# Performance work log

Hardware: AMD Instinct MI355X
Metric: run time of the kernel (lower is better)

The kernel has to match this reference:

```python
import jax, jax.numpy as jnp
import numpy as np

B, L, D_IN, D_OUT = 4, 2048, 4096, 4096


def setup_inputs() -> dict:
    key = jax.random.key(0)
    k1, k2, k3, k4 = jax.random.split(key, 4)
    x = jax.random.normal(k1, (B, L, D_IN), dtype=jnp.float32)
    # base weight stored transposed as [in, out], like self.base = base.T
    base = jax.random.normal(k2, (D_IN, D_OUT), dtype=jnp.float32) * 0.02
    # binary delta sign mask in {0, 1}, stored transposed [in, out]
    mask = jax.random.randint(k3, (D_IN, D_OUT), 0, 2).astype(jnp.int32)
    # coeff = mean(|finetune - base|); a small positive scalar
    coeff = jax.random.uniform(k4, (1,), dtype=jnp.float32) * 0.01
    return {"x": x, "base": base, "coeff": coeff, "mask": mask}


def reference(x, base, coeff, mask):
    # Original: x @ base.T_stored + coeff * (x @ repeated_mask)
    # (t_coeff * x) @ mask == t_coeff * (x @ mask); we avoid materializing the
    # per-batch repeated mask since broadcasting the [in, out] mask is equivalent.
    m = mask.astype(x.dtype)            # {0,1} dequantized mask, [in, out]
    c = coeff[0].astype(x.dtype)
    return jnp.einsum('bld,de->ble', x, base) + c * jnp.einsum('bld,de->ble', x, m)
```

## Files before the change

### kernel.cpp

```cpp
#include <hip/hip_runtime.h>
#include <hip/hip_bf16.h>
#include <stdint.h>

#define DIN 4096
#define DOUT 4096
#define BK 64
#define NT (DIN / BK)

typedef __attribute__((ext_vector_type(8))) short short8;
typedef __attribute__((ext_vector_type(8))) unsigned short ushort8;
typedef __attribute__((ext_vector_type(4))) float f32x4;

__device__ inline unsigned short f2bf(float f) {
    union { float f; unsigned u; } v; v.f = f;
    unsigned r = v.u + 0x7fffu + ((v.u >> 16) & 1u);
    return (unsigned short)(r >> 16);
}

__global__ void cvt_x_kernel(const float* __restrict__ x, ushort* __restrict__ xb, long n8) {
    long i = (long)blockIdx.x * blockDim.x + threadIdx.x;
    if (i >= n8) return;
    const float4* p = (const float4*)(x + i * 8);
    float4 v0 = p[0], v1 = p[1];
    ushort8 o;
    o[0] = f2bf(v0.x); o[1] = f2bf(v0.y); o[2] = f2bf(v0.z); o[3] = f2bf(v0.w);
    o[4] = f2bf(v1.x); o[5] = f2bf(v1.y); o[6] = f2bf(v1.z); o[7] = f2bf(v1.w);
    *(ushort8*)(xb + i * 8) = o;
}

__global__ void make_wt_kernel(const float* __restrict__ base, const int* __restrict__ mask,
                               const float* __restrict__ coeff, ushort* __restrict__ wt) {
    __shared__ float tile[64][65];
    const float c = coeff[0];
    const int t = threadIdx.x;
    const int bd = blockIdx.x >> 6;
    const int be = blockIdx.x & 63;
    const int d0 = bd * 64, e0 = be * 64;
#pragma unroll
    for (int i = 0; i < 4; ++i) {
        int idx = i * 256 + t;
        int r = idx >> 4;
        int c4 = (idx & 15) << 2;
        const float4 bv = *(const float4*)(base + (size_t)(d0 + r) * DOUT + e0 + c4);
        const int4  mv = *(const int4*)(mask + (size_t)(d0 + r) * DOUT + e0 + c4);
        tile[r][c4 + 0] = bv.x + c * (float)mv.x;
        tile[r][c4 + 1] = bv.y + c * (float)mv.y;
        tile[r][c4 + 2] = bv.z + c * (float)mv.z;
        tile[r][c4 + 3] = bv.w + c * (float)mv.w;
    }
    __syncthreads();
#pragma unroll
    for (int i = 0; i < 8; ++i) {
        int idx = i * 256 + t;
        int r = idx >> 5;
        int p = (idx & 31) << 1;
        ushort2 o;
        o.x = f2bf(tile[p][r]);
        o.y = f2bf(tile[p + 1][r]);
        *(ushort2*)(wt + (size_t)(e0 + r) * DIN + d0 + p) = o;
    }
}


#define MFMA(d, va, vb) d = __builtin_amdgcn_mfma_f32_16x16x32_bf16(va, vb, d, 0, 0, 0)

#define MFMA16(AOFF, x0,x1,x2,x3) \
    MFMA(acc[AOFF+0][0],x0,b0); MFMA(acc[AOFF+0][1],x0,b1); MFMA(acc[AOFF+0][2],x0,b2); MFMA(acc[AOFF+0][3],x0,b3); \
    MFMA(acc[AOFF+1][0],x1,b0); MFMA(acc[AOFF+1][1],x1,b1); MFMA(acc[AOFF+1][2],x1,b2); MFMA(acc[AOFF+1][3],x1,b3); \
    MFMA(acc[AOFF+2][0],x2,b0); MFMA(acc[AOFF+2][1],x2,b1); MFMA(acc[AOFF+2][2],x2,b2); MFMA(acc[AOFF+2][3],x2,b3); \
    MFMA(acc[AOFF+3][0],x3,b0); MFMA(acc[AOFF+3][1],x3,b1); MFMA(acc[AOFF+3][2],x3,b2); MFMA(acc[AOFF+3][3],x3,b3);

#define GLL(P, L) \
    __builtin_amdgcn_global_load_lds( \
        (const __attribute__((address_space(1))) void*)(P), \
        (__attribute__((address_space(3))) void*)(L), 16, 0, 0)

#define RDA(BUF,KK,OH,MM) (*(const short8*)&lA[BUF][KK][aoff + (OH)*2048 + (MM)*512])
#define RDB(BUF,KK,NN)    (*(const short8*)&lB[BUF][KK][boff + (NN)*512])

#define STAGE_A(BUF,KK,OFE) { GLL(gA0 + (OFE), &lA[BUF][KK][doff]); \
                              GLL(gA1 + (OFE), &lA[BUF][KK][doff + 4096]); }
#define STAGE_B(BUF,KK,OFE) { GLL(gB0 + (OFE), &lB[BUF][KK][doff]); \
                              GLL(gB1 + (OFE), &lB[BUF][KK][doff + 4096]); }

#define WAITV(N)  asm volatile("s_waitcnt vmcnt(" #N ")" ::: "memory")
#define SBAR      __builtin_amdgcn_s_barrier()

#define KTILE2(BUF, G1, G2, NEXT, OFE1, OFE2) \
  { \
    short8 a0,a1,a2,a3,a4,a5,a6,a7,b0,b1,b2,b3; \
     \
    a0=RDA(BUF,0,0,0); a1=RDA(BUF,0,0,1); a2=RDA(BUF,0,0,2); a3=RDA(BUF,0,0,3); \
    b0=RDB(BUF,0,0);  b1=RDB(BUF,0,1);  b2=RDB(BUF,0,2);  b3=RDB(BUF,0,3); \
    a4=RDA(BUF,0,1,0); a5=RDA(BUF,0,1,1); a6=RDA(BUF,0,1,2); a7=RDA(BUF,0,1,3); \
    if (G1) { STAGE_A(1-(BUF), 1, OFE1) STAGE_B(1-(BUF), 1, OFE1) } \
    SBAR; \
    __builtin_amdgcn_s_setprio(1); \
    MFMA16(0, a0,a1,a2,a3) \
    MFMA16(4, a4,a5,a6,a7) \
    __builtin_amdgcn_s_setprio(0); \
     \
    if (G1) { WAITV(8); } else { WAITV(0); } \
    SBAR; \
     \
    a0=RDA(BUF,1,0,0); a1=RDA(BUF,1,0,1); a2=RDA(BUF,1,0,2); a3=RDA(BUF,1,0,3); \
    b0=RDB(BUF,1,0);  b1=RDB(BUF,1,1);  b2=RDB(BUF,1,2);  b3=RDB(BUF,1,3); \
    a4=RDA(BUF,1,1,0); a5=RDA(BUF,1,1,1); a6=RDA(BUF,1,1,2); a7=RDA(BUF,1,1,3); \
    if (G2) { STAGE_A(BUF, 0, OFE2) STAGE_B(BUF, 0, OFE2) } \
    SBAR; \
    __builtin_amdgcn_s_setprio(1); \
    MFMA16(0, a0,a1,a2,a3) \
    MFMA16(4, a4,a5,a6,a7) \
    __builtin_amdgcn_s_setprio(0); \
     \
    if (G2)        { WAITV(8); } \
    else if (NEXT) { WAITV(4); } \
    SBAR; \
    __builtin_amdgcn_sched_barrier(0); \
  }

__global__ __launch_bounds__(512, 2) void gemm_kernel(const ushort* __restrict__ A,
                                                      const ushort* __restrict__ Bt,
                                                      float* __restrict__ C) {
    __shared__ __align__(16) ushort lA[2][2][256 * 32];
    __shared__ __align__(16) ushort lB[2][2][256 * 32];

    const int tid = threadIdx.x;
    const int lane = tid & 63;
    const int wave = tid >> 6;

    const int nbn = DOUT / 256;
    const int nwg = gridDim.x;
    int bid = blockIdx.x;
    int cpx = nwg >> 3;
    int s = (bid & 7) * cpx + (bid >> 3);
    const int m0 = (s / nbn) * 256;
    const int n0 = (s % nbn) * 256;

    const int wr = wave >> 2;
    const int wc = wave & 3;
    const int fr = lane & 15;
    const int fq = lane >> 4;

    const int st_r = tid >> 2;

    const int sx = ((fr >> 1) & 3) << 3;
    const int aoff = (wr * 128 + fr) * 32 + ((fq << 3) ^ sx);
    const int boff = (wc * 64 + fr) * 32 + ((fq << 3) ^ sx);
    const int doff = tid * 8;
    const int sce = ((tid & 3) << 3) ^ (((st_r >> 1) & 3) << 3);
    const ushort* gA0 = A  + (size_t)(m0 + st_r) * DIN + sce;
    const ushort* gA1 = gA0 + (size_t)128 * DIN;
    const ushort* gB0 = Bt + (size_t)(n0 + st_r) * DIN + sce;
    const ushort* gB1 = gB0 + (size_t)128 * DIN;

    f32x4 acc[8][4] = {};

    STAGE_A(0, 0, 0)   STAGE_B(0, 0, 0)
    STAGE_A(0, 1, 32)  STAGE_B(0, 1, 32)
    STAGE_A(1, 0, 64)  STAGE_B(1, 0, 64)
    WAITV(8);
    SBAR;
    __builtin_amdgcn_sched_barrier(0);

    for (int u = 0; u < NT; u += 2) {
        KTILE2(0, 1, (u + 2 < NT), 1, 96, 128)
        KTILE2(1, (u + 2 < NT), (u + 3 < NT), (u + 2 < NT), 160, 192)
        gA0 += 128; gA1 += 128; gB0 += 128; gB1 += 128;
    }

#pragma unroll
    for (int a = 0; a < 8; ++a) {
        int grow = m0 + wr * 128 + (a >> 2) * 64 + (a & 3) * 16 + fq * 4;
#pragma unroll
        for (int n = 0; n < 4; ++n) {
            int gcol = n0 + wc * 64 + n * 16 + fr;
#pragma unroll
            for (int j = 0; j < 4; ++j)
                C[(size_t)(grow + j) * DOUT + gcol] = acc[a][n][j];
        }
    }
}

extern "C" void kernel_launch(void* const* d_in, const int* in_sizes, int n_in,
                              void* d_out, int out_size, void* d_ws, size_t ws_size,
                              hipStream_t stream) {
    const float* x = (const float*)d_in[0];
    const float* base = (const float*)d_in[1];
    const float* coeff = (const float*)d_in[2];
    const int* mask = (const int*)d_in[3];
    float* out = (float*)d_out;

    const int M = in_sizes[0] / DIN;
    ushort* xb = (ushort*)d_ws;
    ushort* wt = xb + (size_t)M * DIN;

    long n8 = (long)M * DIN / 8;
    cvt_x_kernel<<<(int)((n8 + 255) / 256), 256, 0, stream>>>(x, xb, n8);
    make_wt_kernel<<<(DIN / 64) * (DOUT / 64), 256, 0, stream>>>(base, mask, coeff, wt);

    const int nwg = (M / 256) * (DOUT / 256);
    gemm_kernel<<<nwg, 512, 0, stream>>>(xb, wt, out);
}
```

Baseline: 347.6 us.

## Use 1024-thread GEMM blocks with 16 waves each computing 64x64 subtiles

The GEMM workgroup grows from 512 to 1024 threads (16 waves in a 4x4 grid), so each wave now owns a 64x64 output subtile with half the accumulators. Each thread stages one 16-byte global-to-LDS load per operand per k-slice instead of two, and the vmcnt waits are adjusted to match. The aim is more waves available to hide latency and lower register pressure per wave. In exchange each wave issues fewer MFMAs per LDS fragment read, and launch bounds drop the two-blocks-per-CU hint, so occupancy may not rise.

```diff
diff --git a/kernel.cpp b/kernel.cpp
--- a/kernel.cpp
+++ b/kernel.cpp
@@ -64,64 +64,56 @@
 
 #define MFMA(d, va, vb) d = __builtin_amdgcn_mfma_f32_16x16x32_bf16(va, vb, d, 0, 0, 0)
 
-#define MFMA16(AOFF, x0,x1,x2,x3) \
-    MFMA(acc[AOFF+0][0],x0,b0); MFMA(acc[AOFF+0][1],x0,b1); MFMA(acc[AOFF+0][2],x0,b2); MFMA(acc[AOFF+0][3],x0,b3); \
-    MFMA(acc[AOFF+1][0],x1,b0); MFMA(acc[AOFF+1][1],x1,b1); MFMA(acc[AOFF+1][2],x1,b2); MFMA(acc[AOFF+1][3],x1,b3); \
-    MFMA(acc[AOFF+2][0],x2,b0); MFMA(acc[AOFF+2][1],x2,b1); MFMA(acc[AOFF+2][2],x2,b2); MFMA(acc[AOFF+2][3],x2,b3); \
-    MFMA(acc[AOFF+3][0],x3,b0); MFMA(acc[AOFF+3][1],x3,b1); MFMA(acc[AOFF+3][2],x3,b2); MFMA(acc[AOFF+3][3],x3,b3);
-
 #define GLL(P, L) \
     __builtin_amdgcn_global_load_lds( \
         (const __attribute__((address_space(1))) void*)(P), \
         (__attribute__((address_space(3))) void*)(L), 16, 0, 0)
 
-#define RDA(BUF,KK,OH,MM) (*(const short8*)&lA[BUF][KK][aoff + (OH)*2048 + (MM)*512])
-#define RDB(BUF,KK,NN)    (*(const short8*)&lB[BUF][KK][boff + (NN)*512])
+#define RDA(BUF,KK,MM) (*(const short8*)&lA[BUF][KK][aoff + (MM)*512])
+#define RDB(BUF,KK,NN) (*(const short8*)&lB[BUF][KK][boff + (NN)*512])
 
-#define STAGE_A(BUF,KK,OFE) { GLL(gA0 + (OFE), &lA[BUF][KK][doff]); \
-                              GLL(gA1 + (OFE), &lA[BUF][KK][doff + 4096]); }
-#define STAGE_B(BUF,KK,OFE) { GLL(gB0 + (OFE), &lB[BUF][KK][doff]); \
-                              GLL(gB1 + (OFE), &lB[BUF][KK][doff + 4096]); }
+#define STAGE_A(BUF,KK,OFE) GLL(gA0 + (OFE), &lA[BUF][KK][doff]);
+#define STAGE_B(BUF,KK,OFE) GLL(gB0 + (OFE), &lB[BUF][KK][doff]);
 
 #define WAITV(N)  asm volatile("s_waitcnt vmcnt(" #N ")" ::: "memory")
 #define SBAR      __builtin_amdgcn_s_barrier()
 
-#define KTILE2(BUF, G1, G2, NEXT, OFE1, OFE2) \
+#define MFMA16 \
+    MFMA(acc[0][0],a0,b0); MFMA(acc[0][1],a0,b1); MFMA(acc[0][2],a0,b2); MFMA(acc[0][3],a0,b3); \
+    MFMA(acc[1][0],a1,b0); MFMA(acc[1][1],a1,b1); MFMA(acc[1][2],a1,b2); MFMA(acc[1][3],a1,b3); \
+    MFMA(acc[2][0],a2,b0); MFMA(acc[2][1],a2,b1); MFMA(acc[2][2],a2,b2); MFMA(acc[2][3],a2,b3); \
+    MFMA(acc[3][0],a3,b0); MFMA(acc[3][1],a3,b1); MFMA(acc[3][2],a3,b2); MFMA(acc[3][3],a3,b3);
+
+#define KTILE(BUF, G1, G2, NEXT, OFE1, OFE2) \
   { \
-    short8 a0,a1,a2,a3,a4,a5,a6,a7,b0,b1,b2,b3; \
+    short8 a0,a1,a2,a3,b0,b1,b2,b3; \
      \
-    a0=RDA(BUF,0,0,0); a1=RDA(BUF,0,0,1); a2=RDA(BUF,0,0,2); a3=RDA(BUF,0,0,3); \
-    b0=RDB(BUF,0,0);  b1=RDB(BUF,0,1);  b2=RDB(BUF,0,2);  b3=RDB(BUF,0,3); \
-    a4=RDA(BUF,0,1,0); a5=RDA(BUF,0,1,1); a6=RDA(BUF,0,1,2); a7=RDA(BUF,0,1,3); \
+    a0=RDA(BUF,0,0); a1=RDA(BUF,0,1); a2=RDA(BUF,0,2); a3=RDA(BUF,0,3); \
+    b0=RDB(BUF,0,0); b1=RDB(BUF,0,1); b2=RDB(BUF,0,2); b3=RDB(BUF,0,3); \
     if (G1) { STAGE_A(1-(BUF), 1, OFE1) STAGE_B(1-(BUF), 1, OFE1) } \
+    if (G1) { WAITV(4); } else { WAITV(0); } \
     SBAR; \
     __builtin_amdgcn_s_setprio(1); \
-    MFMA16(0, a0,a1,a2,a3) \
-    MFMA16(4, a4,a5,a6,a7) \
+    MFMA16 \
     __builtin_amdgcn_s_setprio(0); \
      \
-    if (G1) { WAITV(8); } else { WAITV(0); } \
-    SBAR; \
-     \
-    a0=RDA(BUF,1,0,0); a1=RDA(BUF,1,0,1); a2=RDA(BUF,1,0,2); a3=RDA(BUF,1,0,3); \
-    b0=RDB(BUF,1,0);  b1=RDB(BUF,1,1);  b2=RDB(BUF,1,2);  b3=RDB(BUF,1,3); \
-    a4=RDA(BUF,1,1,0); a5=RDA(BUF,1,1,1); a6=RDA(BUF,1,1,2); a7=RDA(BUF,1,1,3); \
+    a0=RDA(BUF,1,0); a1=RDA(BUF,1,1); a2=RDA(BUF,1,2); a3=RDA(BUF,1,3); \
+    b0=RDB(BUF,1,0); b1=RDB(BUF,1,1); b2=RDB(BUF,1,2); b3=RDB(BUF,1,3); \
     if (G2) { STAGE_A(BUF, 0, OFE2) STAGE_B(BUF, 0, OFE2) } \
     SBAR; \
     __builtin_amdgcn_s_setprio(1); \
-    MFMA16(0, a0,a1,a2,a3) \
-    MFMA16(4, a4,a5,a6,a7) \
+    MFMA16 \
     __builtin_amdgcn_s_setprio(0); \
      \
-    if (G2)        { WAITV(8); } \
-    else if (NEXT) { WAITV(4); } \
+    if (G2)        { WAITV(4); } \
+    else if (NEXT) { WAITV(0); } \
     SBAR; \
     __builtin_amdgcn_sched_barrier(0); \
   }
 
-__global__ __launch_bounds__(512, 2) void gemm_kernel(const ushort* __restrict__ A,
-                                                      const ushort* __restrict__ Bt,
-                                                      float* __restrict__ C) {
+__global__ __launch_bounds__(1024) void gemm_kernel(const ushort* __restrict__ A,
+                                                    const ushort* __restrict__ Bt,
+                                                    float* __restrict__ C) {
     __shared__ __align__(16) ushort lA[2][2][256 * 32];
     __shared__ __align__(16) ushort lB[2][2][256 * 32];
 
@@ -142,36 +134,33 @@
     const int fr = lane & 15;
     const int fq = lane >> 4;
 
-    const int st_r = tid >> 2;
-
     const int sx = ((fr >> 1) & 3) << 3;
-    const int aoff = (wr * 128 + fr) * 32 + ((fq << 3) ^ sx);
+    const int aoff = (wr * 64 + fr) * 32 + ((fq << 3) ^ sx);
     const int boff = (wc * 64 + fr) * 32 + ((fq << 3) ^ sx);
     const int doff = tid * 8;
+    const int st_r = tid >> 2;
     const int sce = ((tid & 3) << 3) ^ (((st_r >> 1) & 3) << 3);
     const ushort* gA0 = A  + (size_t)(m0 + st_r) * DIN + sce;
-    const ushort* gA1 = gA0 + (size_t)128 * DIN;
     const ushort* gB0 = Bt + (size_t)(n0 + st_r) * DIN + sce;
-    const ushort* gB1 = gB0 + (size_t)128 * DIN;
 
-    f32x4 acc[8][4] = {};
+    f32x4 acc[4][4] = {};
 
     STAGE_A(0, 0, 0)   STAGE_B(0, 0, 0)
     STAGE_A(0, 1, 32)  STAGE_B(0, 1, 32)
     STAGE_A(1, 0, 64)  STAGE_B(1, 0, 64)
-    WAITV(8);
+    WAITV(4);
     SBAR;
     __builtin_amdgcn_sched_barrier(0);
 
     for (int u = 0; u < NT; u += 2) {
-        KTILE2(0, 1, (u + 2 < NT), 1, 96, 128)
-        KTILE2(1, (u + 2 < NT), (u + 3 < NT), (u + 2 < NT), 160, 192)
-        gA0 += 128; gA1 += 128; gB0 += 128; gB1 += 128;
+        KTILE(0, 1, (u + 2 < NT), 1, 96, 128)
+        KTILE(1, (u + 2 < NT), (u + 3 < NT), (u + 2 < NT), 160, 192)
+        gA0 += 128; gB0 += 128;
     }
 
 #pragma unroll
-    for (int a = 0; a < 8; ++a) {
-        int grow = m0 + wr * 128 + (a >> 2) * 64 + (a & 3) * 16 + fq * 4;
+    for (int a = 0; a < 4; ++a) {
+        int grow = m0 + wr * 64 + a * 16 + fq * 4;
 #pragma unroll
         for (int n = 0; n < 4; ++n) {
             int gcol = n0 + wc * 64 + n * 16 + fr;
@@ -200,5 +189,5 @@
     make_wt_kernel<<<(DIN / 64) * (DOUT / 64), 256, 0, stream>>>(base, mask, coeff, wt);
 
     const int nwg = (M / 256) * (DOUT / 256);
-    gemm_kernel<<<nwg, 512, 0, stream>>>(xb, wt, out);
+    gemm_kernel<<<nwg, 1024, 0, stream>>>(xb, wt, out);
 }
```

Result: slower. 491.2 us (+41.3%).
